# Kernel tuning notes

Hardware: AMD Instinct MI355X
Metric: run time of the kernel (lower is better)

Reference implementation:

```python
import jax, jax.numpy as jnp
import numpy as np

B, N, C, H = 4, 1024, 768, 12
D = C // H
HID = 4 * C
SCALE = D ** -0.5
EPS = 1e-6


def layernorm(x, w, b):
    mu = jnp.mean(x, axis=-1, keepdims=True)
    var = jnp.mean(jnp.square(x - mu), axis=-1, keepdims=True)
    return (x - mu) * jax.lax.rsqrt(var + EPS) * w + b


def setup_inputs() -> dict:
    key = jax.random.key(0)
    ks = jax.random.split(key, 16)
    s = lambda fan_in: 1.0 / np.sqrt(fan_in)
    return {
        "x": jax.random.normal(ks[0], (B, N, C), jnp.float32),
        "physics_bias": jax.random.normal(ks[1], (B, N, N), jnp.float32),
        "qkv_w": jax.random.normal(ks[2], (C, 3 * C), jnp.float32) * s(C),
        "qkv_b": jnp.zeros((3 * C,), jnp.float32),
        "proj_w": jax.random.normal(ks[3], (C, C), jnp.float32) * s(C),
        "proj_b": jnp.zeros((C,), jnp.float32),
        "n1_w": jnp.ones((C,), jnp.float32),
        "n1_b": jnp.zeros((C,), jnp.float32),
        "n2_w": jnp.ones((C,), jnp.float32),
        "n2_b": jnp.zeros((C,), jnp.float32),
        "fc1_w": jax.random.normal(ks[4], (C, HID), jnp.float32) * s(C),
        "fc1_b": jnp.zeros((HID,), jnp.float32),
        "fc2_w": jax.random.normal(ks[5], (HID, C), jnp.float32) * s(HID),
        "fc2_b": jnp.zeros((C,), jnp.float32),
    }


def reference(x, physics_bias, qkv_w, qkv_b, proj_w, proj_b,
              n1_w, n1_b, n2_w, n2_b, fc1_w, fc1_b, fc2_w, fc2_b):
    # --- biased self-attention (pre-norm) ---
    h = layernorm(x, n1_w, n1_b)                         # [B,N,C]
    qkv = (h @ qkv_w + qkv_b).reshape(B, N, 3, H, D)     # [B,N,3,H,D]
    q, k, v = (qkv[:, :, i] for i in range(3))           # each [B,N,H,D]
    attn = jnp.einsum('bnhd,bmhd->bhnm', q, k) * SCALE   # [B,H,N,N]
    attn = attn + physics_bias[:, None, :, :]            # additive physics bias
    attn = jax.nn.softmax(attn, axis=-1)
    o = jnp.einsum('bhnm,bmhd->bnhd', attn, v).reshape(B, N, C)
    x = x + (o @ proj_w + proj_b)
    # --- MLP (pre-norm) ---
    h = layernorm(x, n2_w, n2_b)
    h = jax.nn.gelu(h @ fc1_w + fc1_b, approximate=False)
    x = x + (h @ fc2_w + fc2_b)
    return x
```

## Files before the change

### kernel.cpp

```cpp
#include <hip/hip_runtime.h>
#include <hip/hip_bf16.h>
#include <cstdint>
#include <cstddef>

#define B_   4
#define N_   1024
#define C_   768
#define H_   12
#define D_   64
#define HID_ 3072
#define M_   4096

typedef __attribute__((ext_vector_type(8))) short short8;
typedef __attribute__((ext_vector_type(8))) unsigned short ushort8;
typedef __attribute__((ext_vector_type(4))) unsigned short ubf16x4;
typedef __attribute__((ext_vector_type(4))) float f32x4;

__device__ __forceinline__ void gload16(const void* g, void* l) {
  __builtin_amdgcn_global_load_lds(
      (const __attribute__((address_space(1))) void*)g,
      (__attribute__((address_space(3))) void*)l, 16, 0, 0);
}

__device__ __forceinline__ unsigned short f2bf(float f) {
  __hip_bfloat16 h = __float2bfloat16(f);
  return __builtin_bit_cast(unsigned short, h);
}
__device__ __forceinline__ float bf2f(unsigned short u) {
  unsigned int x = ((unsigned int)u) << 16;
  return __builtin_bit_cast(float, x);
}
__device__ __forceinline__ float ex2(float x) {
  float r;
  asm("v_exp_f32 %0, %1" : "=v"(r) : "v"(x));
  return r;
}
__device__ __forceinline__ float frcp(float x) {
  float r;
  asm("v_rcp_f32 %0, %1" : "=v"(r) : "v"(x));
  return r;
}

__global__ __launch_bounds__(256) void wconv_all(
    const float* __restrict__ qkv_w, const float* __restrict__ proj_w,
    const float* __restrict__ fc1_w, const float* __restrict__ fc2_w,
    unsigned short* __restrict__ wt_qkv, unsigned short* __restrict__ wt_proj,
    unsigned short* __restrict__ wt_fc1, unsigned short* __restrict__ wt_fc2) {
  __shared__ float tile[32][33];
  const int bid = blockIdx.x;
  const float* W;
  unsigned short* Wt;
  int K, Nn, bx, by;
  if (bid < 1728) {
    W = qkv_w; Wt = wt_qkv; K = 768; Nn = 2304;
    bx = bid % 72; by = bid / 72;
  } else if (bid < 1728 + 576) {
    const int i = bid - 1728;
    W = proj_w; Wt = wt_proj; K = 768; Nn = 768;
    bx = i % 24; by = i / 24;
  } else if (bid < 1728 + 576 + 2304) {
    const int i = bid - (1728 + 576);
    W = fc1_w; Wt = wt_fc1; K = 768; Nn = 3072;
    bx = i % 96; by = i / 96;
  } else {
    const int i = bid - (1728 + 576 + 2304);
    W = fc2_w; Wt = wt_fc2; K = 3072; Nn = 768;
    bx = i % 24; by = i / 24;
  }
  const int tx = threadIdx.x & 31, ty = threadIdx.x >> 5;
  const int n0 = bx * 32, k0 = by * 32;
#pragma unroll
  for (int i = 0; i < 32; i += 8)
    tile[ty + i][tx] = W[(size_t)(k0 + ty + i) * Nn + n0 + tx];
  __syncthreads();
#pragma unroll
  for (int i = 0; i < 32; i += 8)
    Wt[(size_t)(n0 + ty + i) * K + k0 + tx] = f2bf(tile[tx][ty + i]);
}

__global__ __launch_bounds__(256) void ln_kernel(const float* __restrict__ x,
                                                 const float* __restrict__ w,
                                                 const float* __restrict__ b,
                                                 unsigned short* __restrict__ out) {
  __shared__ float sbuf[8];
  const int row = blockIdx.x;
  const int t = threadIdx.x;
  const float* xr = x + (size_t)row * C_;
  float v0 = xr[t], v1 = xr[t + 256], v2 = xr[t + 512];
  float s = v0 + v1 + v2;
  float ss = v0 * v0 + v1 * v1 + v2 * v2;
#pragma unroll
  for (int m = 32; m >= 1; m >>= 1) {
    s += __shfl_xor(s, m);
    ss += __shfl_xor(ss, m);
  }
  const int wave = t >> 6, lane = t & 63;
  if (lane == 0) { sbuf[wave] = s; sbuf[4 + wave] = ss; }
  __syncthreads();
  s = sbuf[0] + sbuf[1] + sbuf[2] + sbuf[3];
  ss = sbuf[4] + sbuf[5] + sbuf[6] + sbuf[7];
  const float mu = s * (1.f / C_);
  const float var = ss * (1.f / C_) - mu * mu;
  const float rstd = rsqrtf(var + 1e-6f);
  unsigned short* o = out + (size_t)row * C_;
  o[t]       = f2bf((v0 - mu) * rstd * w[t]       + b[t]);
  o[t + 256] = f2bf((v1 - mu) * rstd * w[t + 256] + b[t + 256]);
  o[t + 512] = f2bf((v2 - mu) * rstd * w[t + 512] + b[t + 512]);
}

template <int MF, bool GELU, bool RES, bool OUTF, bool OUTB>
__global__ __launch_bounds__(256) void gemm_bt(const unsigned short* __restrict__ A,
                                               const unsigned short* __restrict__ Bt,
                                               const float* __restrict__ bias,
                                               const float* __restrict__ res,
                                               float* __restrict__ outF,
                                               unsigned short* __restrict__ outB,
                                               int M, int Nn, int K) {
  __shared__ unsigned short As[3][MF * 32 * 32];
  __shared__ unsigned short Bs[3][128 * 32];
  const int t = threadIdx.x;
  const int lane = t & 63;
  const int wave = t >> 6;
  const int wm = wave >> 1, wn = wave & 1;
  const int r15 = lane & 15, g = lane >> 4;

  constexpr int SPX = (MF == 4) ? 4 : 8;
  constexpr int LGS = (MF == 4) ? 2 : 3;
  const int orig = blockIdx.y * gridDim.x + blockIdx.x;
  const int xcd = orig & 7;
  const int j = orig >> 3;
  const int bm = xcd * SPX + (j & (SPX - 1));
  const int bn = j >> LGS;

  f32x4 acc[MF][4];
#pragma unroll
  for (int m = 0; m < MF; ++m)
#pragma unroll
    for (int n = 0; n < 4; ++n) acc[m][n] = (f32x4){0.f, 0.f, 0.f, 0.f};

  const int srow = t >> 2;
  const int schunk = (t & 3) ^ ((t >> 3) & 3);
  const unsigned short* ga0 = A + (size_t)(bm * (MF * 32) + srow) * K + schunk * 8;
  const unsigned short* gb0 = Bt + (size_t)(bn * 128 + srow) * K + schunk * 8;

#define GSTAGE(kt_, buf_)                                                  \
  {                                                                        \
    const unsigned short* ga = ga0 + (kt_)*32;                             \
    const unsigned short* gb = gb0 + (kt_)*32;                             \
    gload16(ga, (char*)As[buf_] + wave * 1024);                            \
    if constexpr (MF == 4)                                                 \
      gload16(ga + (size_t)64 * K, (char*)As[buf_] + wave * 1024 + 4096);  \
    gload16(gb, (char*)Bs[buf_] + wave * 1024);                            \
    gload16(gb + (size_t)64 * K, (char*)Bs[buf_] + wave * 1024 + 4096);    \
  }

  const int nk = K >> 5;
  GSTAGE(0, 0);
  GSTAGE(1, 1);

  int arow[MF], aoff[MF], boff[4];
#pragma unroll
  for (int m = 0; m < MF; ++m) {
    arow[m] = wm * (MF * 16) + m * 16 + r15;
    aoff[m] = arow[m] * 32 + (g ^ ((arow[m] >> 1) & 3)) * 8;
  }
#pragma unroll
  for (int n = 0; n < 4; ++n) {
    const int rn = wn * 64 + n * 16 + r15;
    boff[n] = rn * 32 + (g ^ ((rn >> 1) & 3)) * 8;
  }

  int rd = 0;
  for (int kt = 0; kt < nk; ++kt) {
    const int rem = nk - kt;
    if (rem >= 2) {
      if constexpr (MF == 4) asm volatile("s_waitcnt vmcnt(4)" ::: "memory");
      else                   asm volatile("s_waitcnt vmcnt(3)" ::: "memory");
    } else {
      asm volatile("s_waitcnt vmcnt(0)" ::: "memory");
    }
    __builtin_amdgcn_s_barrier();

    short8 af[MF], bf[4];
#pragma unroll
    for (int m = 0; m < MF; ++m)
      af[m] = *(const short8*)(As[rd] + aoff[m]);
#pragma unroll
    for (int n = 0; n < 4; ++n)
      bf[n] = *(const short8*)(Bs[rd] + boff[n]);

    if (kt + 2 < nk) {
      const int wr = (rd + 2 >= 3) ? rd - 1 : rd + 2;
      GSTAGE(kt + 2, wr);
    }

    asm volatile("s_waitcnt lgkmcnt(0)" ::: "memory");
    __builtin_amdgcn_sched_barrier(0);
    __builtin_amdgcn_s_setprio(1);
#pragma unroll
    for (int m = 0; m < MF; ++m)
#pragma unroll
      for (int n = 0; n < 4; ++n)
        acc[m][n] = __builtin_amdgcn_mfma_f32_16x16x32_bf16(af[m], bf[n], acc[m][n], 0, 0, 0);
    __builtin_amdgcn_s_setprio(0);
    rd = (rd == 2) ? 0 : rd + 1;
  }
#undef GSTAGE

#pragma unroll
  for (int m = 0; m < MF; ++m) {
#pragma unroll
    for (int n = 0; n < 4; ++n) {
#pragma unroll
      for (int r = 0; r < 4; ++r) {
        const int row = bm * (MF * 32) + wm * (MF * 16) + m * 16 + g * 4 + r;
        const int col = bn * 128 + wn * 64 + n * 16 + r15;
        float v = acc[m][n][r] + bias[col];
        if (GELU) v = 0.5f * v * (1.f + erff(v * 0.70710678118654752f));
        if (RES) v += res[(size_t)row * Nn + col];
        if (OUTF) outF[(size_t)row * Nn + col] = v;
        if (OUTB) outB[(size_t)row * Nn + col] = f2bf(v);
      }
    }
  }
}

__global__ __launch_bounds__(256) void attn_kernel(const unsigned short* __restrict__ qkv,
                                                   const float* __restrict__ pbias,
                                                   unsigned short* __restrict__ o) {
  __shared__ unsigned short Ks[2][64 * 64];
  __shared__ unsigned short Vt[2][64 * 64];
  __shared__ unsigned short Ps[4][16 * 64];
  const int t = threadIdx.x, lane = t & 63, wave = t >> 6;
  const int bh = blockIdx.y;
  const int b = bh / H_, h = bh % H_;
  const int q0 = blockIdx.x * 64;
  const int r15 = lane & 15, g = lane >> 4;
  const int qrow = q0 + wave * 16;
  const float LOG2E = 1.44269504088896f;
  const float QS = 0.125f * 1.44269504088896f;
  const int NT = N_ / 64;

  short8 aq[2];
  {
    const unsigned short* qp =
        qkv + (size_t)(b * N_ + qrow + r15) * (3 * C_) + h * D_ + g * 8;
    const ushort8 r0 = *(const ushort8*)qp;
    const ushort8 r1 = *(const ushort8*)(qp + 32);
#pragma unroll
    for (int jj = 0; jj < 8; ++jj) {
      aq[0][jj] = (short)f2bf(bf2f(r0[jj]) * QS);
      aq[1][jj] = (short)f2bf(bf2f(r1[jj]) * QS);
    }
  }
  short8 ones;
#pragma unroll
  for (int jj = 0; jj < 8; ++jj) ones[jj] = (short)0x3F80;

  f32x4 oacc[4], lacc;
#pragma unroll
  for (int n = 0; n < 4; ++n) oacc[n] = (f32x4){0.f, 0.f, 0.f, 0.f};
  lacc = (f32x4){0.f, 0.f, 0.f, 0.f};
  float m_run = -1e30f;

  const unsigned short* kbase = qkv + (size_t)b * N_ * (3 * C_) + C_ + h * D_;
  const unsigned short* vbase = qkv + (size_t)b * N_ * (3 * C_) + 2 * C_ + h * D_;

  const float* bp = pbias + (size_t)b * N_ * N_ + (size_t)(qrow + r15) * N_;

  const int krow = t >> 3;
  const int kchunk = (t & 7) ^ (krow & 7);
  const int vp = t & 31;
  const int vq = t >> 5;
  const int vkey = vp * 2, vd0 = vq * 8;

#define KSTAGE(kb_, nb_)                                                       \
  {                                                                            \
    const unsigned short* kg =                                                 \
        kbase + (size_t)((kb_)*64 + krow) * (3 * C_) + kchunk * 8;             \
    gload16(kg, (char*)Ks[nb_] + wave * 1024);                                 \
    gload16(kg + (size_t)32 * (3 * C_), (char*)Ks[nb_] + wave * 1024 + 4096);  \
  }

#define VWRITE(nb_, va_, vb_)                                                        \
  {                                                                                  \
    char* vdst = (char*)Vt[nb_];                                                     \
    _Pragma("unroll") for (int jj = 0; jj < 8; ++jj) {                               \
      const int d = vd0 + jj;                                                        \
      const unsigned int pack =                                                      \
          (unsigned int)(va_)[jj] | ((unsigned int)(vb_)[jj] << 16);                 \
      *(unsigned int*)(vdst + d * 128 + (((vp >> 2) ^ (d & 7)) << 4) +               \
                       (vp & 3) * 4) = pack;                                         \
    }                                                                                \
  }

  KSTAGE(0, 0);
  {
    const unsigned short* vg = vbase + (size_t)vkey * (3 * C_) + vd0;
    const ushort8 va0 = *(const ushort8*)vg;
    const ushort8 vb0 = *(const ushort8*)(vg + 3 * C_);
    VWRITE(0, va0, vb0);
  }
  f32x4 bcur[4], bnext[4];
#pragma unroll
  for (int n = 0; n < 4; ++n)
    bcur[n] = *(const f32x4*)(bp + n * 16 + g * 4);

  for (int kb = 0; kb < NT; ++kb) {
    const int cur = kb & 1;
    __syncthreads();

    ushort8 va, vb2;
    const bool more = (kb + 1 < NT);
    if (more) {
      KSTAGE(kb + 1, cur ^ 1);
      const unsigned short* vg =
          vbase + (size_t)((kb + 1) * 64 + vkey) * (3 * C_) + vd0;
      va = *(const ushort8*)vg;
      vb2 = *(const ushort8*)(vg + 3 * C_);
#pragma unroll
      for (int n = 0; n < 4; ++n)
        bnext[n] = *(const f32x4*)(bp + 64 + n * 16 + g * 4);
    }
    bp += 64;

    const unsigned short* Ksc = Ks[cur];
    f32x4 sacc[4];
#pragma unroll
    for (int n = 0; n < 4; ++n) sacc[n] = (f32x4){0.f, 0.f, 0.f, 0.f};
    __builtin_amdgcn_s_setprio(1);
#pragma unroll
    for (int kk = 0; kk < 2; ++kk) {
#pragma unroll
      for (int n = 0; n < 4; ++n) {
        short8 bk = *(const short8*)(Ksc + (n * 16 + r15) * 64 +
                                     (((kk * 4 + g) ^ (r15 & 7)) << 3));
        sacc[n] = __builtin_amdgcn_mfma_f32_16x16x32_bf16(bk, aq[kk], sacc[n], 0, 0, 0);
      }
    }
    __builtin_amdgcn_s_setprio(0);

    float p[4][4];
    float tm = -3e38f;
#pragma unroll
    for (int n = 0; n < 4; ++n)
#pragma unroll
      for (int r = 0; r < 4; ++r) {
        p[n][r] = fmaf(bcur[n][r], LOG2E, sacc[n][r]);
        tm = fmaxf(tm, p[n][r]);
      }
    tm = fmaxf(tm, __shfl_xor(tm, 16));
    tm = fmaxf(tm, __shfl_xor(tm, 32));
    const int need = (tm > m_run + 8.0f);
    if (__any(need)) {
      const float mn = fmaxf(m_run, tm);
      const float corr = ex2(m_run - mn);
      m_run = mn;
      float cr[4];
#pragma unroll
      for (int r = 0; r < 4; ++r) cr[r] = __shfl(corr, g * 4 + r);
#pragma unroll
      for (int r = 0; r < 4; ++r) {
        lacc[r] *= cr[r];
#pragma unroll
        for (int n = 0; n < 4; ++n) oacc[n][r] *= cr[r];
      }
    }
#pragma unroll
    for (int n = 0; n < 4; ++n)
#pragma unroll
      for (int r = 0; r < 4; ++r) p[n][r] = ex2(p[n][r] - m_run);

    unsigned short* Psw = Ps[wave];
#pragma unroll
    for (int n = 0; n < 4; ++n) {
      ubf16x4 pk;
#pragma unroll
      for (int r = 0; r < 4; ++r) pk[r] = f2bf(p[n][r]);
      const int chunk = (2 * n + (g >> 1)) ^ (r15 & 7);
      *(ubf16x4*)(Psw + r15 * 64 + chunk * 8 + (g & 1) * 4) = pk;
    }

    const unsigned short* Vtc = Vt[cur];
    __builtin_amdgcn_s_setprio(1);
#pragma unroll
    for (int kk = 0; kk < 2; ++kk) {
      short8 ap = *(const short8*)(Psw + r15 * 64 + (((kk * 4 + g) ^ (r15 & 7)) << 3));
      lacc = __builtin_amdgcn_mfma_f32_16x16x32_bf16(ap, ones, lacc, 0, 0, 0);
#pragma unroll
      for (int n = 0; n < 4; ++n) {
        short8 bv = *(const short8*)(Vtc + (n * 16 + r15) * 64 +
                                     (((kk * 4 + g) ^ (r15 & 7)) << 3));
        oacc[n] = __builtin_amdgcn_mfma_f32_16x16x32_bf16(ap, bv, oacc[n], 0, 0, 0);
      }
    }
    __builtin_amdgcn_s_setprio(0);

    if (more) {
      VWRITE(cur ^ 1, va, vb2);
#pragma unroll
      for (int n = 0; n < 4; ++n) bcur[n] = bnext[n];
    }
  }
#undef KSTAGE
#undef VWRITE

  float rl[4];
#pragma unroll
  for (int r = 0; r < 4; ++r) rl[r] = frcp(lacc[r]);
#pragma unroll
  for (int n = 0; n < 4; ++n) {
#pragma unroll
    for (int r = 0; r < 4; ++r) {
      const int row = qrow + g * 4 + r;
      const float v = oacc[n][r] * rl[r];
      o[(size_t)(b * N_ + row) * C_ + h * D_ + n * 16 + r15] = f2bf(v);
    }
  }
}

extern "C" void kernel_launch(void* const* d_in, const int* in_sizes, int n_in,
                              void* d_out, int out_size, void* d_ws, size_t ws_size,
                              hipStream_t stream) {
  const float* x      = (const float*)d_in[0];
  const float* pbias  = (const float*)d_in[1];
  const float* qkv_w  = (const float*)d_in[2];
  const float* qkv_b  = (const float*)d_in[3];
  const float* proj_w = (const float*)d_in[4];
  const float* proj_b = (const float*)d_in[5];
  const float* n1_w   = (const float*)d_in[6];
  const float* n1_b   = (const float*)d_in[7];
  const float* n2_w   = (const float*)d_in[8];
  const float* n2_b   = (const float*)d_in[9];
  const float* fc1_w  = (const float*)d_in[10];
  const float* fc1_b  = (const float*)d_in[11];
  const float* fc2_w  = (const float*)d_in[12];
  const float* fc2_b  = (const float*)d_in[13];
  float* out = (float*)d_out;

  char* ws = (char*)d_ws;
  unsigned short* wt_qkv  = (unsigned short*)(ws + 0);
  unsigned short* wt_proj = (unsigned short*)(ws + 3538944);
  unsigned short* wt_fc1  = (unsigned short*)(ws + 4718592);
  unsigned short* wt_fc2  = (unsigned short*)(ws + 9437184);
  float*          x2      = (float*)(ws + 14155776);
  unsigned short* h1      = (unsigned short*)(ws + 26738688);
  unsigned short* qkvb    = (unsigned short*)(ws + 33030144);

  wconv_all<<<1728 + 576 + 2304 + 2304, 256, 0, stream>>>(
      qkv_w, proj_w, fc1_w, fc2_w, wt_qkv, wt_proj, wt_fc1, wt_fc2);

  ln_kernel<<<M_, 256, 0, stream>>>(x, n1_w, n1_b, h1);
  gemm_bt<4, false, false, false, true><<<dim3(32, 18), 256, 0, stream>>>(
      h1, wt_qkv, qkv_b, nullptr, nullptr, qkvb, M_, 3 * C_, C_);
  attn_kernel<<<dim3(N_ / 64, B_ * H_), 256, 0, stream>>>(qkvb, pbias, h1);
  gemm_bt<2, false, true, true, false><<<dim3(64, 6), 256, 0, stream>>>(
      h1, wt_proj, proj_b, x, x2, nullptr, M_, C_, C_);
  ln_kernel<<<M_, 256, 0, stream>>>(x2, n2_w, n2_b, h1);
  gemm_bt<4, true, false, false, true><<<dim3(32, 24), 256, 0, stream>>>(
      h1, wt_fc1, fc1_b, nullptr, nullptr, qkvb, M_, HID_, C_);
  gemm_bt<2, false, true, true, false><<<dim3(64, 6), 256, 0, stream>>>(
      qkvb, wt_fc2, fc2_b, x2, out, nullptr, M_, C_, HID_);
}
```

Measured before the change: 178.8 us.

## Prefetch physics bias two tiles ahead with ping-pong registers and manual waitcnt

The attention inner loop is unrolled by two, and the physics-bias loads are double-buffered in registers (biasA/biasB) so each tile's bias is fetched two iterations ahead, after the scores have been consumed. __syncthreads is replaced by explicit lgkmcnt/vmcnt waits plus s_barrier, so outstanding bias loads are not forced to drain at the barrier. Sched barriers pin where the prefetch is issued. The P tile store changes from packed 4-element writes to scalar 2-byte writes. The goal is to hide the HBM latency of the large fp32 bias stream, at the cost of more LDS store instructions and a fragile vmcnt count that depends on how many loads are in flight.

```diff
diff --git a/kernel.cpp b/kernel.cpp
--- a/kernel.cpp
+++ b/kernel.cpp
@@ -13,7 +13,6 @@
 
 typedef __attribute__((ext_vector_type(8))) short short8;
 typedef __attribute__((ext_vector_type(8))) unsigned short ushort8;
-typedef __attribute__((ext_vector_type(4))) unsigned short ubf16x4;
 typedef __attribute__((ext_vector_type(4))) float f32x4;
 
 __device__ __forceinline__ void gload16(const void* g, void* l) {
@@ -265,8 +264,7 @@
 
   const unsigned short* kbase = qkv + (size_t)b * N_ * (3 * C_) + C_ + h * D_;
   const unsigned short* vbase = qkv + (size_t)b * N_ * (3 * C_) + 2 * C_ + h * D_;
-
-  const float* bp = pbias + (size_t)b * N_ * N_ + (size_t)(qrow + r15) * N_;
+  const float* bq = pbias + (size_t)b * N_ * N_ + (size_t)(qrow + r15) * N_;
 
   const int krow = t >> 3;
   const int kchunk = (t & 7) ^ (krow & 7);
@@ -295,113 +293,111 @@
   }
 
   KSTAGE(0, 0);
+  f32x4 biasA[4], biasB[4];
   {
     const unsigned short* vg = vbase + (size_t)vkey * (3 * C_) + vd0;
     const ushort8 va0 = *(const ushort8*)vg;
     const ushort8 vb0 = *(const ushort8*)(vg + 3 * C_);
+#pragma unroll
+    for (int n = 0; n < 4; ++n) biasA[n] = *(const f32x4*)(bq + n * 16 + g * 4);
+#pragma unroll
+    for (int n = 0; n < 4; ++n) biasB[n] = *(const f32x4*)(bq + 64 + n * 16 + g * 4);
     VWRITE(0, va0, vb0);
   }
-  f32x4 bcur[4], bnext[4];
-#pragma unroll
-  for (int n = 0; n < 4; ++n)
-    bcur[n] = *(const f32x4*)(bp + n * 16 + g * 4);
-
-  for (int kb = 0; kb < NT; ++kb) {
-    const int cur = kb & 1;
-    __syncthreads();
-
-    ushort8 va, vb2;
-    const bool more = (kb + 1 < NT);
-    if (more) {
-      KSTAGE(kb + 1, cur ^ 1);
-      const unsigned short* vg =
-          vbase + (size_t)((kb + 1) * 64 + vkey) * (3 * C_) + vd0;
-      va = *(const ushort8*)vg;
-      vb2 = *(const ushort8*)(vg + 3 * C_);
-#pragma unroll
-      for (int n = 0; n < 4; ++n)
-        bnext[n] = *(const f32x4*)(bp + 64 + n * 16 + g * 4);
-    }
-    bp += 64;
-
-    const unsigned short* Ksc = Ks[cur];
-    f32x4 sacc[4];
-#pragma unroll
-    for (int n = 0; n < 4; ++n) sacc[n] = (f32x4){0.f, 0.f, 0.f, 0.f};
-    __builtin_amdgcn_s_setprio(1);
-#pragma unroll
-    for (int kk = 0; kk < 2; ++kk) {
-#pragma unroll
-      for (int n = 0; n < 4; ++n) {
-        short8 bk = *(const short8*)(Ksc + (n * 16 + r15) * 64 +
-                                     (((kk * 4 + g) ^ (r15 & 7)) << 3));
-        sacc[n] = __builtin_amdgcn_mfma_f32_16x16x32_bf16(bk, aq[kk], sacc[n], 0, 0, 0);
-      }
-    }
-    __builtin_amdgcn_s_setprio(0);
-
-    float p[4][4];
-    float tm = -3e38f;
-#pragma unroll
-    for (int n = 0; n < 4; ++n)
-#pragma unroll
-      for (int r = 0; r < 4; ++r) {
-        p[n][r] = fmaf(bcur[n][r], LOG2E, sacc[n][r]);
-        tm = fmaxf(tm, p[n][r]);
-      }
-    tm = fmaxf(tm, __shfl_xor(tm, 16));
-    tm = fmaxf(tm, __shfl_xor(tm, 32));
-    const int need = (tm > m_run + 8.0f);
-    if (__any(need)) {
-      const float mn = fmaxf(m_run, tm);
-      const float corr = ex2(m_run - mn);
-      m_run = mn;
-      float cr[4];
-#pragma unroll
-      for (int r = 0; r < 4; ++r) cr[r] = __shfl(corr, g * 4 + r);
-#pragma unroll
-      for (int r = 0; r < 4; ++r) {
-        lacc[r] *= cr[r];
-#pragma unroll
-        for (int n = 0; n < 4; ++n) oacc[n][r] *= cr[r];
-      }
-    }
-#pragma unroll
-    for (int n = 0; n < 4; ++n)
-#pragma unroll
-      for (int r = 0; r < 4; ++r) p[n][r] = ex2(p[n][r] - m_run);
-
-    unsigned short* Psw = Ps[wave];
-#pragma unroll
-    for (int n = 0; n < 4; ++n) {
-      ubf16x4 pk;
-#pragma unroll
-      for (int r = 0; r < 4; ++r) pk[r] = f2bf(p[n][r]);
-      const int chunk = (2 * n + (g >> 1)) ^ (r15 & 7);
-      *(ubf16x4*)(Psw + r15 * 64 + chunk * 8 + (g & 1) * 4) = pk;
-    }
-
-    const unsigned short* Vtc = Vt[cur];
-    __builtin_amdgcn_s_setprio(1);
-#pragma unroll
-    for (int kk = 0; kk < 2; ++kk) {
-      short8 ap = *(const short8*)(Psw + r15 * 64 + (((kk * 4 + g) ^ (r15 & 7)) << 3));
-      lacc = __builtin_amdgcn_mfma_f32_16x16x32_bf16(ap, ones, lacc, 0, 0, 0);
-#pragma unroll
-      for (int n = 0; n < 4; ++n) {
-        short8 bv = *(const short8*)(Vtc + (n * 16 + r15) * 64 +
-                                     (((kk * 4 + g) ^ (r15 & 7)) << 3));
-        oacc[n] = __builtin_amdgcn_mfma_f32_16x16x32_bf16(ap, bv, oacc[n], 0, 0, 0);
-      }
-    }
-    __builtin_amdgcn_s_setprio(0);
-
-    if (more) {
-      VWRITE(cur ^ 1, va, vb2);
-#pragma unroll
-      for (int n = 0; n < 4; ++n) bcur[n] = bnext[n];
-    }
-  }
+
+#define ABODY(kb_, BS)                                                             \
+  {                                                                                \
+    const int cur_ = (kb_)&1;                                                      \
+    asm volatile("s_waitcnt lgkmcnt(0)" ::: "memory");                             \
+    asm volatile("s_waitcnt vmcnt(4)" ::: "memory");                               \
+    __builtin_amdgcn_s_barrier();                                                  \
+    ushort8 va, vb2;                                                               \
+    const bool more = (kb_) + 1 < NT;                                              \
+    if (more) {                                                                    \
+      KSTAGE((kb_) + 1, cur_ ^ 1);                                                 \
+      const unsigned short* vg =                                                   \
+          vbase + (size_t)(((kb_) + 1) * 64 + vkey) * (3 * C_) + vd0;              \
+      va = *(const ushort8*)vg;                                                    \
+      vb2 = *(const ushort8*)(vg + 3 * C_);                                        \
+    }                                                                              \
+    const unsigned short* Ksc = Ks[cur_];                                          \
+    f32x4 sacc[4];                                                                 \
+    _Pragma("unroll") for (int n = 0; n < 4; ++n)                                  \
+        sacc[n] = (f32x4){0.f, 0.f, 0.f, 0.f};                                     \
+    __builtin_amdgcn_s_setprio(1);                                                 \
+    _Pragma("unroll") for (int kk = 0; kk < 2; ++kk) {                             \
+      _Pragma("unroll") for (int n = 0; n < 4; ++n) {                              \
+        short8 bk = *(const short8*)(Ksc + (n * 16 + r15) * 64 +                   \
+                                     (((kk * 4 + g) ^ (r15 & 7)) << 3));           \
+        sacc[n] =                                                                  \
+            __builtin_amdgcn_mfma_f32_16x16x32_bf16(bk, aq[kk], sacc[n], 0, 0, 0); \
+      }                                                                            \
+    }                                                                              \
+    __builtin_amdgcn_s_setprio(0);                                                 \
+    float p[4][4];                                                                 \
+    float tm = -3e38f;                                                             \
+    _Pragma("unroll") for (int n = 0; n < 4; ++n) {                                \
+      _Pragma("unroll") for (int r = 0; r < 4; ++r) {                              \
+        p[n][r] = fmaf(BS[n][r], LOG2E, sacc[n][r]);                               \
+        tm = fmaxf(tm, p[n][r]);                                                   \
+      }                                                                            \
+    }                                                                              \
+    __builtin_amdgcn_sched_barrier(0);                                             \
+    {                                                                              \
+      const float* bsrc = bq + (((kb_) + 2 < NT ? (kb_) + 2 : NT - 1) << 6);       \
+      _Pragma("unroll") for (int n = 0; n < 4; ++n)                                \
+          BS[n] = *(const f32x4*)(bsrc + n * 16 + g * 4);                          \
+    }                                                                              \
+    __builtin_amdgcn_sched_barrier(0);                                             \
+    tm = fmaxf(tm, __shfl_xor(tm, 16));                                            \
+    tm = fmaxf(tm, __shfl_xor(tm, 32));                                            \
+    const int need = (tm > m_run + 8.0f);                                          \
+    if (__any(need)) {                                                             \
+      const float mn = fmaxf(m_run, tm);                                           \
+      const float corr = ex2(m_run - mn);                                          \
+      m_run = mn;                                                                  \
+      float cr[4];                                                                 \
+      _Pragma("unroll") for (int r = 0; r < 4; ++r)                                \
+          cr[r] = __shfl(corr, g * 4 + r);                                         \
+      _Pragma("unroll") for (int r = 0; r < 4; ++r) {                              \
+        lacc[r] *= cr[r];                                                          \
+        _Pragma("unroll") for (int n = 0; n < 4; ++n) oacc[n][r] *= cr[r];         \
+      }                                                                            \
+    }                                                                              \
+    _Pragma("unroll") for (int n = 0; n < 4; ++n) {                                \
+      _Pragma("unroll") for (int r = 0; r < 4; ++r)                                \
+          p[n][r] = ex2(p[n][r] - m_run);                                          \
+    }                                                                              \
+    unsigned short* Psw = Ps[wave];                                                \
+    _Pragma("unroll") for (int n = 0; n < 4; ++n) {                                \
+      _Pragma("unroll") for (int r = 0; r < 4; ++r) {                              \
+        const int col = n * 16 + g * 4 + r;                                        \
+        Psw[r15 * 64 + (((col >> 3) ^ (r15 & 7)) << 3) + (col & 7)] =              \
+            f2bf(p[n][r]);                                                         \
+      }                                                                            \
+    }                                                                              \
+    const unsigned short* Vtc = Vt[cur_];                                          \
+    __builtin_amdgcn_s_setprio(1);                                                 \
+    _Pragma("unroll") for (int kk = 0; kk < 2; ++kk) {                             \
+      short8 ap =                                                                  \
+          *(const short8*)(Psw + r15 * 64 + (((kk * 4 + g) ^ (r15 & 7)) << 3));    \
+      lacc = __builtin_amdgcn_mfma_f32_16x16x32_bf16(ap, ones, lacc, 0, 0, 0);     \
+      _Pragma("unroll") for (int n = 0; n < 4; ++n) {                              \
+        short8 bv = *(const short8*)(Vtc + (n * 16 + r15) * 64 +                   \
+                                     (((kk * 4 + g) ^ (r15 & 7)) << 3));           \
+        oacc[n] =                                                                  \
+            __builtin_amdgcn_mfma_f32_16x16x32_bf16(ap, bv, oacc[n], 0, 0, 0);     \
+      }                                                                            \
+    }                                                                              \
+    __builtin_amdgcn_s_setprio(0);                                                 \
+    if (more) { VWRITE(cur_ ^ 1, va, vb2); }                                       \
+  }
+
+  for (int kb2 = 0; kb2 < NT; kb2 += 2) {
+    ABODY(kb2, biasA);
+    ABODY(kb2 + 1, biasB);
+  }
+#undef ABODY
 #undef KSTAGE
 #undef VWRITE
 
```

Result: no change. 180.9 us (+1.2%).
